# Performance work log

Measured on AMD Instinct MI355X. Metric: run time of the kernel, lower is better.

Reference implementation:

```python
import jax, jax.numpy as jnp
import numpy as np

B, C, H, W = 16, 256, 64, 64
HID, N, SD, NH, HD, NC = 256, 300, 64, 4, 16, 80


def _conv1x1(x, w, b):
    # x: (B,Cin,H,W), w: (Cout,Cin)
    return jnp.einsum('bchw,oc->bohw', x, w) + b[None, :, None, None]


def _lin(x, w, b):
    return x @ w.T + b


def _ln(x, g, b, eps=1e-5):
    mu = x.mean(-1, keepdims=True)
    var = ((x - mu) ** 2).mean(-1, keepdims=True)
    return (x - mu) / jnp.sqrt(var + eps) * g + b


def setup_inputs() -> dict:
    key = jax.random.key(0)
    ks = jax.random.split(key, 16)
    def w(k, shape, s=0.02):
        return jax.random.normal(k, shape, jnp.float32) * s
    return {
        'x': jax.random.normal(ks[0], (B, C, H, W), jnp.float32),
        'spotlight_sources': w(ks[1], (N, SD)),
        'pos_w': w(ks[2], (HID // 2, 2)), 'pos_b': jnp.zeros((HID // 2,), jnp.float32),
        'fp_w': w(ks[3], (HID, C)), 'fp_b': jnp.zeros((HID,), jnp.float32),
        'bn_g': jnp.ones((HID,), jnp.float32), 'bn_b': jnp.zeros((HID,), jnp.float32),
        'bn_m': jnp.zeros((HID,), jnp.float32), 'bn_v': jnp.ones((HID,), jnp.float32),
        'key_w': w(ks[4], (SD, HID)), 'key_b': jnp.zeros((SD,), jnp.float32),
        'val_w': w(ks[5], (HID, HID)), 'val_b': jnp.zeros((HID,), jnp.float32),
        'ctp_w': w(ks[6], (NC, HID)), 'ctp_b': jnp.zeros((NC,), jnp.float32),
        'bb1_w': w(ks[7], (HID, HID)), 'bb1_b': jnp.zeros((HID,), jnp.float32),
        'bbln_g': jnp.ones((HID,), jnp.float32), 'bbln_b': jnp.zeros((HID,), jnp.float32),
        'bb2_w': w(ks[8], (HID // 2, HID)), 'bb2_b': jnp.zeros((HID // 2,), jnp.float32),
        'bb3_w': w(ks[9], (4, HID // 2)), 'bb3_b': jnp.zeros((4,), jnp.float32),
        'ch1_w': w(ks[10], (HID, HID)), 'ch1_b': jnp.zeros((HID,), jnp.float32),
        'chln_g': jnp.ones((HID,), jnp.float32), 'chln_b': jnp.zeros((HID,), jnp.float32),
        'ch2_w': w(ks[11], (HID // 2, HID)), 'ch2_b': jnp.zeros((HID // 2,), jnp.float32),
        'ch3_w': w(ks[12], (1, HID // 2)), 'ch3_b': jnp.zeros((1,), jnp.float32),
    }


def _forward(x, spotlight_sources, pos_w, pos_b, fp_w, fp_b, bn_g, bn_b, bn_m, bn_v,
             key_w, key_b, val_w, val_b, ctp_w, ctp_b,
             bb1_w, bb1_b, bbln_g, bbln_b, bb2_w, bb2_b, bb3_w, bb3_b,
             ch1_w, ch1_b, chln_g, chln_b, ch2_w, ch2_b, ch3_w, ch3_b):
    Bv, _, Hh, Ww = x.shape
    # position encoding: 2-channel normalized (y, x) grid, conv1x1 to HID//2
    y = jnp.linspace(-1.0, 1.0, Hh, dtype=jnp.float32)
    xc = jnp.linspace(-1.0, 1.0, Ww, dtype=jnp.float32)
    coords = jnp.stack([jnp.broadcast_to(y[:, None], (Hh, Ww)),
                        jnp.broadcast_to(xc[None, :], (Hh, Ww))], 0)[None]  # (1,2,H,W)
    # feature_proj: conv1x1 + BatchNorm(eval) + ReLU
    feats = _conv1x1(x, fp_w, fp_b)
    feats = (feats - bn_m[None, :, None, None]) / jnp.sqrt(bn_v[None, :, None, None] + 1e-5)
    feats = jax.nn.relu(feats * bn_g[None, :, None, None] + bn_b[None, :, None, None])
    pos = jnp.broadcast_to(_conv1x1(coords, pos_w, pos_b), (Bv, HID // 2, Hh, Ww))
    comb = jnp.concatenate([feats[:, :HID // 2], pos], axis=1)  # (B,HID,H,W)
    keys = _conv1x1(comb, key_w, key_b).reshape(Bv, NH, HD, Hh * Ww)   # (B,h,d,M)
    vals = _conv1x1(comb, val_w, val_b).reshape(Bv, HID, Hh * Ww)      # (B,HID,M)
    q = spotlight_sources.reshape(N, NH, HD)                            # (N,h,d)
    logits = jnp.einsum('nhd,bhdm->bhnm', q, keys) / jnp.sqrt(jnp.float32(HD))
    attn = jax.nn.softmax(logits, axis=-1).mean(axis=1)                 # (B,N,M), head-averaged
    maps = attn.reshape(Bv, N, Hh, Ww)
    sf = jnp.einsum('bnm,bcm->bnc', attn, vals)                         # (B,N,HID)
    def head(z, w1, b1, g, bb, w2, b2, w3, b3):
        z = jax.nn.relu(_ln(_lin(z, w1, b1), g, bb))
        z = jax.nn.relu(_lin(z, w2, b2))
        return _lin(z, w3, b3)
    boxes = head(sf, bb1_w, bb1_b, bbln_g, bbln_b, bb2_w, bb2_b, bb3_w, bb3_b)
    scores = jax.nn.sigmoid(head(sf, ch1_w, ch1_b, chln_g, chln_b, ch2_w, ch2_b, ch3_w, ch3_b))
    cls = _lin(sf, ctp_w, ctp_b)
    # diversity loss: mean off-diagonal cosine similarity of attention rows
    an = attn / jnp.maximum(jnp.linalg.norm(attn, axis=2, keepdims=True), 1e-12)
    sim = jnp.einsum('bnm,bkm->bnk', an, an)
    div = (sim.sum() - jnp.einsum('bnn->', sim)) / (N * (N - 1)) * 0.1
    return boxes, scores, cls, maps, div, sf


def reference(x, spotlight_sources, pos_w, pos_b, fp_w, fp_b, bn_g, bn_b, bn_m, bn_v,
              key_w, key_b, val_w, val_b, ctp_w, ctp_b,
              bb1_w, bb1_b, bbln_g, bbln_b, bb2_w, bb2_b, bb3_w, bb3_b,
              ch1_w, ch1_b, chln_g, chln_b, ch2_w, ch2_b, ch3_w, ch3_b):
    return _forward(x, spotlight_sources, pos_w, pos_b, fp_w, fp_b, bn_g, bn_b, bn_m, bn_v,
                    key_w, key_b, val_w, val_b, ctp_w, ctp_b,
                    bb1_w, bb1_b, bbln_g, bbln_b, bb2_w, bb2_b, bb3_w, bb3_b,
                    ch1_w, ch1_b, chln_g, chln_b, ch2_w, ch2_b, ch3_w, ch3_b)
```

## Files before the change

### kernel.cpp

```cpp
#include <hip/hip_runtime.h>
#include <math.h>

#define BB 16
#define CIN 256
#define MM 4096
#define HIDC 256
#define NQ 300
#define NHH 4
#define HDD 16

#define OFF_BOXES  0
#define OFF_SCORES 19200
#define OFF_CLS    24000
#define OFF_MAPS   408000
#define OFF_DIV    20068800
#define OFF_SF     20068801

#define WS_COMB16  0
#define WS_KEYS16  8388608
#define WS_ATTN16  10485760
#define WS_T16     21544960
#define WS_VALW16  22159360
#define WS_SUMS    22192128
#define WS_NORM    22211328
#define WS_ACC     22216128
#define WS_P       22216192

#define HP_SF16   (WS_P + 0)
#define HP_Z2BB   (WS_P + 2457600)
#define HP_Z2CH   (WS_P + 2764800)
#define HP_HW     (WS_P + 3072000)
#define WS_B2     (WS_P + 3180544)
#define WS_Q16    (WS_P + 3200000)
#define WS_XT     25426432
#define WS_COMBT  33815040
#define WS_FPW16  42203648
#define WS_KEYW16 42220032
#define WS_Z1PRE2 42228224
#define WS_Z1B16  44685824

#define HW_BB1 0
#define HW_CH1 65536
#define HW_BB2 131072
#define HW_CH2 163840
#define HW_CTP 196608

typedef short short8 __attribute__((ext_vector_type(8)));
typedef float floatx4 __attribute__((ext_vector_type(4)));

__device__ __forceinline__ unsigned short f2bf(float f){
  unsigned int u = __float_as_uint(f);
  u = (u + 0x7FFFu + ((u >> 16) & 1u)) >> 16;
  return (unsigned short)u;
}
__device__ __forceinline__ float bf1(unsigned short u){
  return __uint_as_float((unsigned int)u << 16);
}

__global__ __launch_bounds__(256) void zero4_kernel(float4* __restrict__ p, int n4){
  int i = blockIdx.x * 256 + threadIdx.x;
  if (i < n4) p[i] = make_float4(0.f, 0.f, 0.f, 0.f);
}

__global__ __launch_bounds__(256) void init_kernel(const float* __restrict__ ss,
    const float* __restrict__ fp_w, const float* __restrict__ key_w,
    unsigned short* __restrict__ q16, unsigned short* __restrict__ fpw16,
    unsigned short* __restrict__ keyw16){
  int i = blockIdx.x * 256 + threadIdx.x;
  int T = gridDim.x * 256;
  for (int j = i; j < 320*64; j += T)
    q16[j] = (j < NQ*64) ? f2bf(ss[j] * 0.25f) : (unsigned short)0;
  for (int j = i; j < 128*256; j += T) fpw16[j] = f2bf(fp_w[j]);
  for (int j = i; j < 64*256; j += T)  keyw16[j] = f2bf(key_w[j]);
}

__global__ __launch_bounds__(256) void cast_heads_kernel(
    const float* __restrict__ val_w, const float* __restrict__ bb1_w,
    const float* __restrict__ ch1_w, const float* __restrict__ bb2_w,
    const float* __restrict__ ch2_w, const float* __restrict__ ctp_w,
    const float* __restrict__ bb2_b, const float* __restrict__ ch2_b,
    unsigned short* __restrict__ valw16, unsigned short* __restrict__ hw16,
    float* __restrict__ b2){
  int i = blockIdx.x * 256 + threadIdx.x;
  int T = gridDim.x * 256;
  for (int j = i; j < 65536; j += T) valw16[j] = f2bf(val_w[j]);
  for (int j = i; j < 65536; j += T) hw16[HW_BB1 + j] = f2bf(bb1_w[j]);
  for (int j = i; j < 65536; j += T) hw16[HW_CH1 + j] = f2bf(ch1_w[j]);
  for (int j = i; j < 32768; j += T) hw16[HW_BB2 + j] = f2bf(bb2_w[j]);
  for (int j = i; j < 32768; j += T) hw16[HW_CH2 + j] = f2bf(ch2_w[j]);
  for (int j = i; j < 20480; j += T) hw16[HW_CTP + j] = f2bf(ctp_w[j]);
  for (int j = i; j < 128; j += T){ b2[j] = bb2_b[j]; b2[128 + j] = ch2_b[j]; }
}

__global__ __launch_bounds__(256) void pos_kernel(const float* __restrict__ pos_w,
                                                  const float* __restrict__ pos_b,
                                                  unsigned short* __restrict__ comb16,
                                                  unsigned short* __restrict__ combT){
  int lin = blockIdx.x * 256 + threadIdx.x;
  if (lin < 2097152){
    int m  = (lin & 1023) * 4;
    int c  = (lin >> 10) & 127;
    int b  = lin >> 17;
    int row = m >> 6, col = m & 63;
    float y  = -1.f + 2.f * (float)row / 63.f;
    float wy = pos_w[c*2], wx = pos_w[c*2+1], pb = pos_b[c];
    float base = wy * y + pb;
    ushort4 u;
    u.x = f2bf(base + wx * (-1.f + 2.f * (float)(col+0) / 63.f));
    u.y = f2bf(base + wx * (-1.f + 2.f * (float)(col+1) / 63.f));
    u.z = f2bf(base + wx * (-1.f + 2.f * (float)(col+2) / 63.f));
    u.w = f2bf(base + wx * (-1.f + 2.f * (float)(col+3) / 63.f));
    *(ushort4*)&comb16[((size_t)(b*HIDC + 128 + c))*MM + m] = u;
  } else if (lin < 2097152 + 131072){
    int l2 = lin - 2097152;
    int c4 = (l2 & 31) * 4;
    int m  = l2 >> 5;
    int row = m >> 6, col = m & 63;
    float y = -1.f + 2.f * (float)row / 63.f;
    float x = -1.f + 2.f * (float)col / 63.f;
    ushort4 u;
    u.x = f2bf(pos_w[(c4+0)*2] * y + pos_w[(c4+0)*2+1] * x + pos_b[c4+0]);
    u.y = f2bf(pos_w[(c4+1)*2] * y + pos_w[(c4+1)*2+1] * x + pos_b[c4+1]);
    u.z = f2bf(pos_w[(c4+2)*2] * y + pos_w[(c4+2)*2+1] * x + pos_b[c4+2]);
    u.w = f2bf(pos_w[(c4+3)*2] * y + pos_w[(c4+3)*2+1] * x + pos_b[c4+3]);
    #pragma unroll
    for (int b = 0; b < BB; b++)
      *(ushort4*)&combT[((size_t)b*MM + m)*CIN + 128 + c4] = u;
  }
}

__global__ __launch_bounds__(256) void transpose_x_kernel(
    const float* __restrict__ in, unsigned short* __restrict__ outp){
  int b = blockIdx.z;
  int m0 = blockIdx.x * 64;
  int r0 = blockIdx.y * 64;
  __shared__ unsigned short lds[64][68];
  int t = threadIdx.x;
  const float* ib = in + (size_t)b * CIN * MM;
  #pragma unroll
  for (int j = 0; j < 4; j++){
    int lin = j*256 + t;
    int rr = lin >> 4;
    int m4 = (lin & 15) * 4;
    float4 v = *(const float4*)&ib[(size_t)(r0 + rr)*MM + m0 + m4];
    lds[m4+0][rr] = f2bf(v.x);
    lds[m4+1][rr] = f2bf(v.y);
    lds[m4+2][rr] = f2bf(v.z);
    lds[m4+3][rr] = f2bf(v.w);
  }
  __syncthreads();
  unsigned short* ob = outp + (size_t)b * MM * CIN;
  #pragma unroll
  for (int j = 0; j < 4; j++){
    int lin = j*256 + t;
    int mm = lin >> 4;
    int c4 = (lin & 15) * 4;
    ushort4 u;
    u.x = lds[mm][c4+0]; u.y = lds[mm][c4+1];
    u.z = lds[mm][c4+2]; u.w = lds[mm][c4+3];
    *(ushort4*)&ob[(size_t)(m0 + mm)*CIN + r0 + c4] = u;
  }
}

__global__ __launch_bounds__(64) void comb_mfma_kernel(
    const unsigned short* __restrict__ fpw16, const unsigned short* __restrict__ xT16,
    const float* __restrict__ fp_b, const float* __restrict__ bn_g,
    const float* __restrict__ bn_b, const float* __restrict__ bn_m,
    const float* __restrict__ bn_v, unsigned short* __restrict__ comb16,
    unsigned short* __restrict__ combT){
  int b = blockIdx.z;
  const unsigned short* Bb = xT16 + (size_t)b * MM * CIN;
  unsigned short* cb  = comb16 + (size_t)b * HIDC * MM;
  unsigned short* cTb = combT + (size_t)b * MM * CIN;
  int lane = threadIdx.x;
  int r16 = lane & 15;
  int ko  = (lane >> 4) * 8;
  const unsigned short* arow[4];
  const unsigned short* brow[4];
  #pragma unroll
  for (int i = 0; i < 4; i++){
    arow[i] = fpw16 + (size_t)(blockIdx.y*64 + i*16 + r16) * CIN + ko;
    brow[i] = Bb + (size_t)(blockIdx.x*64 + i*16 + r16) * CIN + ko;
  }
  floatx4 acc[4][4];
  #pragma unroll
  for (int i = 0; i < 4; i++)
    #pragma unroll
    for (int j = 0; j < 4; j++)
      acc[i][j] = (floatx4){0.f, 0.f, 0.f, 0.f};
  short8 a[4], bv[4], a2[4], b2[4];
  #pragma unroll
  for (int i = 0; i < 4; i++){
    a[i]  = *(const short8*)(arow[i]);
    bv[i] = *(const short8*)(brow[i]);
  }
  for (int k = 32; k < CIN; k += 32){
    #pragma unroll
    for (int i = 0; i < 4; i++){
      a2[i] = *(const short8*)(arow[i] + k);
      b2[i] = *(const short8*)(brow[i] + k);
    }
    #pragma unroll
    for (int i = 0; i < 4; i++)
      #pragma unroll
      for (int j = 0; j < 4; j++)
        acc[i][j] = __builtin_amdgcn_mfma_f32_16x16x32_bf16(a[i], bv[j], acc[i][j], 0, 0, 0);
    #pragma unroll
    for (int i = 0; i < 4; i++){ a[i] = a2[i]; bv[i] = b2[i]; }
  }
  #pragma unroll
  for (int i = 0; i < 4; i++)
    #pragma unroll
    for (int j = 0; j < 4; j++)
      acc[i][j] = __builtin_amdgcn_mfma_f32_16x16x32_bf16(a[i], bv[j], acc[i][j], 0, 0, 0);
  int cq = lane & 15, rq = (lane >> 4) * 4;
  #pragma unroll
  for (int i = 0; i < 4; i++){
    int rbase = blockIdx.y*64 + i*16 + rq;
    float mul[4], ofs[4];
    #pragma unroll
    for (int reg = 0; reg < 4; reg++){
      int rr = rbase + reg;
      float sc = rsqrtf(bn_v[rr] + 1e-5f);
      mul[reg] = sc * bn_g[rr];
      ofs[reg] = (fp_b[rr] - bn_m[rr]) * mul[reg] + bn_b[rr];
    }
    #pragma unroll
    for (int j = 0; j < 4; j++){
      int cc = blockIdx.x*64 + j*16 + cq;
      ushort4 u;
      float v0 = fmaxf(acc[i][j][0] * mul[0] + ofs[0], 0.f); u.x = f2bf(v0);
      float v1 = fmaxf(acc[i][j][1] * mul[1] + ofs[1], 0.f); u.y = f2bf(v1);
      float v2 = fmaxf(acc[i][j][2] * mul[2] + ofs[2], 0.f); u.z = f2bf(v2);
      float v3 = fmaxf(acc[i][j][3] * mul[3] + ofs[3], 0.f); u.w = f2bf(v3);
      cb[(size_t)(rbase+0) * MM + cc] = u.x;
      cb[(size_t)(rbase+1) * MM + cc] = u.y;
      cb[(size_t)(rbase+2) * MM + cc] = u.z;
      cb[(size_t)(rbase+3) * MM + cc] = u.w;
      *(ushort4*)&cTb[(size_t)cc * CIN + rbase] = u;
    }
  }
}


__global__ __launch_bounds__(256) void attn_sums_kernel(
    const unsigned short* __restrict__ q16, const unsigned short* __restrict__ keysT,
    float* __restrict__ sums){
  int b = blockIdx.z, ny = blockIdx.y, mx = blockIdx.x;
  int tid = threadIdx.x, w = tid >> 6, lane = tid & 63;
  int n0 = ny * 64;
  int l15 = lane & 15, qh = lane >> 4;
  int ko = (qh & 1) * 8;
  bool lo = lane < 32;
  const unsigned short* kT = keysT + (size_t)b * MM * 64;
  int mwb = mx*128 + w*32;
  __shared__ unsigned short qlds[64][72];
  __shared__ float spart[4][NHH][64];
  for (int c = tid; c < 512; c += 256){
    int r = c >> 3, d8 = (c & 7) * 8;
    *(short8*)&qlds[r][d8] = *(const short8*)&q16[(size_t)(n0 + r)*64 + d8];
  }
  __syncthreads();
  short8 zz = {0,0,0,0,0,0,0,0};
  #pragma unroll 1
  for (int h = 0; h < NHH; h++){
    short8 bq[4];
    #pragma unroll
    for (int ni = 0; ni < 4; ni++)
      bq[ni] = lo ? *(const short8*)&qlds[ni*16 + l15][h*16 + ko] : zz;
    float sacc[4] = {0.f, 0.f, 0.f, 0.f};
    #pragma unroll
    for (int ms = 0; ms < 2; ms++){
      int m = mwb + ms*16 + l15;
      short8 a = lo ? *(const short8*)&kT[(size_t)m*64 + h*16 + ko] : zz;
      #pragma unroll
      for (int ni = 0; ni < 4; ni++){
        floatx4 l = __builtin_amdgcn_mfma_f32_16x16x32_bf16(a, bq[ni],
                        (floatx4){0.f,0.f,0.f,0.f}, 0, 0, 0);
        sacc[ni] += __expf(l[0]) + __expf(l[1]) + __expf(l[2]) + __expf(l[3]);
      }
    }
    #pragma unroll
    for (int ni = 0; ni < 4; ni++){
      float v = sacc[ni];
      v += __shfl_xor(v, 16); v += __shfl_xor(v, 32);
      if (lane < 16) spart[w][h][ni*16 + lane] = v;
    }
  }
  __syncthreads();
  if (tid < NHH*64){
    int h = tid >> 6, r = tid & 63, n = n0 + r;
    if (n < NQ){
      float v = spart[0][h][r] + spart[1][h][r] + spart[2][h][r] + spart[3][h][r];
      atomicAdd(&sums[((size_t)b*NHH + h)*NQ + n], v);
    }
  }
}

__global__ __launch_bounds__(256) void attn_emit_kernel(
    const unsigned short* __restrict__ q16, const unsigned short* __restrict__ keysT,
    const float* __restrict__ sums, float* __restrict__ maps,
    unsigned short* __restrict__ attn16, float* __restrict__ norms){
  int b = blockIdx.z, ny = blockIdx.y, mx = blockIdx.x;
  int tid = threadIdx.x, w = tid >> 6, lane = tid & 63;
  int n0 = ny * 64;
  int l15 = lane & 15, qh = lane >> 4;
  int ko = (qh & 1) * 8;
  bool lo = lane < 32;
  __shared__ unsigned short qlds[64][72];
  __shared__ float inv_s[NHH][64];
  __shared__ float npart[4][64];
  for (int c = tid; c < 512; c += 256){
    int r = c >> 3, d8 = (c & 7) * 8;
    *(short8*)&qlds[r][d8] = *(const short8*)&q16[(size_t)(n0 + r)*64 + d8];
  }
  if (tid < NHH*64){
    int h = tid >> 6, r = tid & 63, n = n0 + r;
    inv_s[h][r] = (n < NQ) ? 0.25f / sums[((size_t)b*NHH + h)*NQ + n] : 0.f;
  }
  __syncthreads();
  const unsigned short* kT = keysT + (size_t)b * MM * 64;
  int mwb = mx*128 + w*32;
  short8 zz = {0,0,0,0,0,0,0,0};
  float nacc[4] = {0.f, 0.f, 0.f, 0.f};
  float* mb = maps + (size_t)b * NQ * MM;
  unsigned short* ab = attn16 + (size_t)b * NQ * MM;
  #pragma unroll 1
  for (int ms = 0; ms < 2; ms++){
    asm volatile("" ::: "memory");
    int mbase = mwb + ms*16;
    int mk = mbase + l15;
    floatx4 o[4];
    #pragma unroll
    for (int ni = 0; ni < 4; ni++) o[ni] = (floatx4){0.f,0.f,0.f,0.f};
    #pragma unroll
    for (int h = 0; h < NHH; h++){
      short8 a = lo ? *(const short8*)&kT[(size_t)mk*64 + h*16 + ko] : zz;
      #pragma unroll
      for (int ni = 0; ni < 4; ni++){
        short8 bq = lo ? *(const short8*)&qlds[ni*16 + l15][h*16 + ko] : zz;
        floatx4 l = __builtin_amdgcn_mfma_f32_16x16x32_bf16(a, bq,
                        (floatx4){0.f,0.f,0.f,0.f}, 0, 0, 0);
        float iv = inv_s[h][ni*16 + l15];
        o[ni][0] += __expf(l[0]) * iv;
        o[ni][1] += __expf(l[1]) * iv;
        o[ni][2] += __expf(l[2]) * iv;
        o[ni][3] += __expf(l[3]) * iv;
      }
    }
    #pragma unroll
    for (int ni = 0; ni < 4; ni++){
      nacc[ni] += o[ni][0]*o[ni][0] + o[ni][1]*o[ni][1]
                + o[ni][2]*o[ni][2] + o[ni][3]*o[ni][3];
      int n = n0 + ni*16 + l15;
      if (n < NQ){
        size_t off = (size_t)n*MM + mbase + qh*4;
        float4 v; v.x = o[ni][0]; v.y = o[ni][1]; v.z = o[ni][2]; v.w = o[ni][3];
        *(float4*)&mb[off] = v;
        ushort4 u;
        u.x = f2bf(v.x); u.y = f2bf(v.y); u.z = f2bf(v.z); u.w = f2bf(v.w);
        *(ushort4*)&ab[off] = u;
      }
    }
  }
  #pragma unroll
  for (int ni = 0; ni < 4; ni++){
    float v = nacc[ni];
    v += __shfl_xor(v, 16); v += __shfl_xor(v, 32);
    if (lane < 16) npart[w][ni*16 + lane] = v;
  }
  __syncthreads();
  if (tid < 64){
    int n = n0 + tid;
    if (n < NQ){
      float v = npart[0][tid] + npart[1][tid] + npart[2][tid] + npart[3][tid];
      atomicAdd(&norms[(size_t)b*NQ + n], v);
    }
  }
}

template<bool RELU>
__global__ __launch_bounds__(64) void mfma_nt_kernel(
    const unsigned short* __restrict__ A, size_t sA,
    const unsigned short* __restrict__ B, size_t sB,
    const float* __restrict__ bias, int bstride,
    float* __restrict__ C, unsigned short* __restrict__ C16,
    size_t sC, int ldc, int Mr, int Nc, int K){
  int bz = blockIdx.z;
  const unsigned short* Ab = A + (size_t)bz * sA;
  const unsigned short* Bb = B + (size_t)bz * sB;
  int lane = threadIdx.x;
  int r16 = lane & 15;
  int ko  = (lane >> 4) * 8;
  const unsigned short* arow[4];
  const unsigned short* brow[4];
  #pragma unroll
  for (int i = 0; i < 4; i++){
    int m = blockIdx.y*64 + i*16 + r16;
    if (m > Mr - 1) m = Mr - 1;
    arow[i] = Ab + (size_t)m * K + ko;
    int n = blockIdx.x*64 + i*16 + r16;
    if (n > Nc - 1) n = Nc - 1;
    brow[i] = Bb + (size_t)n * K + ko;
  }
  floatx4 acc[4][4];
  #pragma unroll
  for (int i = 0; i < 4; i++)
    #pragma unroll
    for (int j = 0; j < 4; j++)
      acc[i][j] = (floatx4){0.f, 0.f, 0.f, 0.f};
  short8 a[4], bv[4], a2[4], b2[4];
  #pragma unroll
  for (int i = 0; i < 4; i++){
    a[i]  = *(const short8*)(arow[i]);
    bv[i] = *(const short8*)(brow[i]);
  }
  for (int k = 32; k < K; k += 32){
    #pragma unroll
    for (int i = 0; i < 4; i++){
      a2[i] = *(const short8*)(arow[i] + k);
      b2[i] = *(const short8*)(brow[i] + k);
    }
    #pragma unroll
    for (int i = 0; i < 4; i++)
      #pragma unroll
      for (int j = 0; j < 4; j++)
        acc[i][j] = __builtin_amdgcn_mfma_f32_16x16x32_bf16(a[i], bv[j], acc[i][j], 0, 0, 0);
    #pragma unroll
    for (int i = 0; i < 4; i++){ a[i] = a2[i]; bv[i] = b2[i]; }
  }
  #pragma unroll
  for (int i = 0; i < 4; i++)
    #pragma unroll
    for (int j = 0; j < 4; j++)
      acc[i][j] = __builtin_amdgcn_mfma_f32_16x16x32_bf16(a[i], bv[j], acc[i][j], 0, 0, 0);
  int cq = lane & 15, rq = (lane >> 4) * 4;
  #pragma unroll
  for (int j = 0; j < 4; j++){
    int cc = blockIdx.x*64 + j*16 + cq;
    if (cc >= Nc) continue;
    float bv_ = bias ? bias[bz*bstride + cc] : 0.f;
    #pragma unroll
    for (int i = 0; i < 4; i++){
      int rbase = blockIdx.y*64 + i*16 + rq;
      #pragma unroll
      for (int reg = 0; reg < 4; reg++){
        int rr = rbase + reg;
        if (rr < Mr){
          float v = acc[i][j][reg] + bv_;
          if (RELU) v = fmaxf(v, 0.f);
          size_t o = (size_t)bz * sC + (size_t)rr * ldc + cc;
          if (C)   C[o] = v;
          if (C16) C16[o] = f2bf(v);
        }
      }
    }
  }
}

__global__ __launch_bounds__(256) void mfma_red4_kernel(
    const unsigned short* __restrict__ A, size_t sA,
    const unsigned short* __restrict__ B, size_t sB,
    unsigned short* __restrict__ C16, size_t sC, int ldc, int Mr, int K){
  int bz = blockIdx.z;
  int tid = threadIdx.x, w = tid >> 6, lane = tid & 63;
  int kchunk = K >> 2;
  const unsigned short* Ab = A + (size_t)bz * sA + (size_t)w * kchunk;
  const unsigned short* Bb = B + (size_t)bz * sB + (size_t)w * kchunk;
  int r16 = lane & 15;
  int ko  = (lane >> 4) * 8;
  const unsigned short* arow[4];
  const unsigned short* brow[4];
  #pragma unroll
  for (int i = 0; i < 4; i++){
    int m = blockIdx.y*64 + i*16 + r16;
    if (m > Mr - 1) m = Mr - 1;
    arow[i] = Ab + (size_t)m * K + ko;
    int n = blockIdx.x*64 + i*16 + r16;
    brow[i] = Bb + (size_t)n * K + ko;
  }
  floatx4 acc[4][4];
  #pragma unroll
  for (int i = 0; i < 4; i++)
    #pragma unroll
    for (int j = 0; j < 4; j++)
      acc[i][j] = (floatx4){0.f, 0.f, 0.f, 0.f};
  short8 a[4], bv[4], a2[4], b2[4];
  #pragma unroll
  for (int i = 0; i < 4; i++){
    a[i]  = *(const short8*)(arow[i]);
    bv[i] = *(const short8*)(brow[i]);
  }
  for (int k = 32; k < kchunk; k += 32){
    #pragma unroll
    for (int i = 0; i < 4; i++){
      a2[i] = *(const short8*)(arow[i] + k);
      b2[i] = *(const short8*)(brow[i] + k);
    }
    #pragma unroll
    for (int i = 0; i < 4; i++)
      #pragma unroll
      for (int j = 0; j < 4; j++)
        acc[i][j] = __builtin_amdgcn_mfma_f32_16x16x32_bf16(a[i], bv[j], acc[i][j], 0, 0, 0);
    #pragma unroll
    for (int i = 0; i < 4; i++){ a[i] = a2[i]; bv[i] = b2[i]; }
  }
  #pragma unroll
  for (int i = 0; i < 4; i++)
    #pragma unroll
    for (int j = 0; j < 4; j++)
      acc[i][j] = __builtin_amdgcn_mfma_f32_16x16x32_bf16(a[i], bv[j], acc[i][j], 0, 0, 0);
  __shared__ float red[64][65];
  int cq = lane & 15, rq = (lane >> 4) * 4;
  #pragma unroll 1
  for (int ph = 0; ph < 4; ph++){
    if (w == ph){
      #pragma unroll
      for (int i = 0; i < 4; i++)
        #pragma unroll
        for (int reg = 0; reg < 4; reg++){
          int r = i*16 + rq + reg;
          #pragma unroll
          for (int j = 0; j < 4; j++){
            int c = j*16 + cq;
            if (ph == 0) red[r][c] = acc[i][j][reg];
            else         red[r][c] += acc[i][j][reg];
          }
        }
    }
    __syncthreads();
  }
  unsigned short* Cb = C16 + (size_t)bz * sC;
  for (int idx = tid; idx < 1024; idx += 256){
    int r = idx >> 4, c4 = (idx & 15) * 4;
    int gr = blockIdx.y*64 + r;
    if (gr < Mr){
      ushort4 u;
      u.x = f2bf(red[r][c4+0]); u.y = f2bf(red[r][c4+1]);
      u.z = f2bf(red[r][c4+2]); u.w = f2bf(red[r][c4+3]);
      *(ushort4*)&Cb[(size_t)gr * ldc + blockIdx.x*64 + c4] = u;
    }
  }
}

__global__ __launch_bounds__(256) void ln_relu2_kernel(const float* __restrict__ zin,
    const float* __restrict__ bias_b, const float* __restrict__ bias_c,
    const float* __restrict__ g_b, const float* __restrict__ be_b,
    const float* __restrict__ g_c, const float* __restrict__ be_c,
    unsigned short* __restrict__ zout){
  int z = blockIdx.y;
  const float* bias = z ? bias_c : bias_b;
  const float* g    = z ? g_c : g_b;
  const float* be   = z ? be_c : be_b;
  const float* zi = zin + (size_t)z * 1228800;
  unsigned short* zo = zout + (size_t)z * 1228800;
  int row = blockIdx.x * 4 + (threadIdx.x >> 6);
  int lane = threadIdx.x & 63;
  float4 v = *(const float4*)&zi[(size_t)row * 256 + lane * 4];
  float4 bi = *(const float4*)&bias[lane * 4];
  v.x += bi.x; v.y += bi.y; v.z += bi.z; v.w += bi.w;
  float s = v.x + v.y + v.z + v.w;
  #pragma unroll
  for (int off = 32; off >= 1; off >>= 1) s += __shfl_xor(s, off);
  float mean = s * (1.f/256.f);
  float dx = v.x - mean, dy = v.y - mean, dz = v.z - mean, dw = v.w - mean;
  float sq = dx*dx + dy*dy + dz*dz + dw*dw;
  #pragma unroll
  for (int off = 32; off >= 1; off >>= 1) sq += __shfl_xor(sq, off);
  float inv = rsqrtf(sq * (1.f/256.f) + 1e-5f);
  float4 gv = *(const float4*)&g[lane * 4];
  float4 bb = *(const float4*)&be[lane * 4];
  ushort4 u;
  u.x = f2bf(fmaxf(dx*inv*gv.x + bb.x, 0.f));
  u.y = f2bf(fmaxf(dy*inv*gv.y + bb.y, 0.f));
  u.z = f2bf(fmaxf(dz*inv*gv.z + bb.z, 0.f));
  u.w = f2bf(fmaxf(dw*inv*gv.w + bb.w, 0.f));
  *(ushort4*)&zo[(size_t)row * 256 + lane * 4] = u;
}

__global__ __launch_bounds__(256) void head3_kernel(
    const unsigned short* __restrict__ z2bb, const unsigned short* __restrict__ z2ch,
    const float* __restrict__ bb3_w, const float* __restrict__ bb3_b,
    const float* __restrict__ ch3_w, const float* __restrict__ ch3_b,
    float* __restrict__ boxes, float* __restrict__ scores){
  int row = blockIdx.x * 4 + (threadIdx.x >> 6);
  int lane = threadIdx.x & 63;
  float zb0 = bf1(z2bb[(size_t)row*128 + 2*lane]);
  float zb1 = bf1(z2bb[(size_t)row*128 + 2*lane + 1]);
  float zc0 = bf1(z2ch[(size_t)row*128 + 2*lane]);
  float zc1 = bf1(z2ch[(size_t)row*128 + 2*lane + 1]);
  float acc[5];
  #pragma unroll
  for (int o = 0; o < 4; o++)
    acc[o] = bb3_w[o*128 + 2*lane]*zb0 + bb3_w[o*128 + 2*lane + 1]*zb1;
  acc[4] = ch3_w[2*lane]*zc0 + ch3_w[2*lane + 1]*zc1;
  #pragma unroll
  for (int o = 0; o < 5; o++){
    float v = acc[o];
    #pragma unroll
    for (int off = 32; off >= 1; off >>= 1) v += __shfl_xor(v, off);
    acc[o] = v;
  }
  if (lane == 0){
    #pragma unroll
    for (int o = 0; o < 4; o++)
      boxes[(size_t)row*4 + o] = acc[o] + bb3_b[o];
    float sv = acc[4] + ch3_b[0];
    scores[row] = 1.f / (1.f + __expf(-sv));
  }
}

__global__ __launch_bounds__(256) void simdiv_kernel(const unsigned short* __restrict__ attn16,
    const float* __restrict__ norms, float* __restrict__ acc){
  int b = blockIdx.y;
  int m = blockIdx.x * 256 + threadIdx.x;
  __shared__ float inv_s[NQ];
  __shared__ float red[4];
  for (int i = threadIdx.x; i < NQ; i += 256)
    inv_s[i] = 1.f / fmaxf(sqrtf(norms[(size_t)b * NQ + i]), 1e-12f);
  __syncthreads();
  const unsigned short* ab = attn16 + (size_t)b * NQ * MM;
  float S = 0.f;
  for (int n = 0; n < NQ; n++)
    S += bf1(ab[(size_t)n * MM + m]) * inv_s[n];
  float p = S * S;
  #pragma unroll
  for (int off = 32; off >= 1; off >>= 1) p += __shfl_xor(p, off);
  int w = threadIdx.x >> 6, lane = threadIdx.x & 63;
  if (lane == 0) red[w] = p;
  __syncthreads();
  if (threadIdx.x == 0) atomicAdd(acc, red[0] + red[1] + red[2] + red[3]);
}

__global__ void finalize_kernel(const float* __restrict__ acc, float* __restrict__ out_div){
  out_div[0] = (acc[0] - (float)(BB * NQ)) / (float)(NQ * (NQ - 1)) * 0.1f;
}

extern "C" void kernel_launch(void* const* d_in, const int* in_sizes, int n_in,
                              void* d_out, int out_size, void* d_ws, size_t ws_size,
                              hipStream_t stream){
  const float* x      = (const float*)d_in[0];
  const float* ss     = (const float*)d_in[1];
  const float* pos_w  = (const float*)d_in[2];
  const float* pos_b  = (const float*)d_in[3];
  const float* fp_w   = (const float*)d_in[4];
  const float* fp_b   = (const float*)d_in[5];
  const float* bn_g   = (const float*)d_in[6];
  const float* bn_b   = (const float*)d_in[7];
  const float* bn_m   = (const float*)d_in[8];
  const float* bn_v   = (const float*)d_in[9];
  const float* key_w  = (const float*)d_in[10];
  const float* key_b  = (const float*)d_in[11];
  const float* val_w  = (const float*)d_in[12];
  const float* val_b  = (const float*)d_in[13];
  const float* ctp_w  = (const float*)d_in[14];
  const float* ctp_b  = (const float*)d_in[15];
  const float* bb1_w  = (const float*)d_in[16];
  const float* bb1_b  = (const float*)d_in[17];
  const float* bbln_g = (const float*)d_in[18];
  const float* bbln_b = (const float*)d_in[19];
  const float* bb2_w  = (const float*)d_in[20];
  const float* bb2_b  = (const float*)d_in[21];
  const float* bb3_w  = (const float*)d_in[22];
  const float* bb3_b  = (const float*)d_in[23];
  const float* ch1_w  = (const float*)d_in[24];
  const float* ch1_b  = (const float*)d_in[25];
  const float* chln_g = (const float*)d_in[26];
  const float* chln_b = (const float*)d_in[27];
  const float* ch2_w  = (const float*)d_in[28];
  const float* ch2_b  = (const float*)d_in[29];
  const float* ch3_w  = (const float*)d_in[30];
  const float* ch3_b  = (const float*)d_in[31];

  float* out    = (float*)d_out;
  float* boxes  = out + OFF_BOXES;
  float* scores = out + OFF_SCORES;
  float* cls    = out + OFF_CLS;
  float* maps   = out + OFF_MAPS;
  float* divp   = out + OFF_DIV;
  float* sfout  = out + OFF_SF;

  float* ws = (float*)d_ws;
  unsigned short* comb16 = (unsigned short*)(ws + WS_COMB16);
  unsigned short* keysT  = (unsigned short*)(ws + WS_KEYS16);
  unsigned short* attn16 = (unsigned short*)(ws + WS_ATTN16);
  unsigned short* t16    = (unsigned short*)(ws + WS_T16);
  unsigned short* valw16 = (unsigned short*)(ws + WS_VALW16);
  float* sums  = ws + WS_SUMS;
  float* norms = ws + WS_NORM;
  float* dacc  = ws + WS_ACC;
  unsigned short* sf16   = (unsigned short*)(ws + HP_SF16);
  unsigned short* z2bb16 = (unsigned short*)(ws + HP_Z2BB);
  unsigned short* z2ch16 = (unsigned short*)(ws + HP_Z2CH);
  unsigned short* hw16   = (unsigned short*)(ws + HP_HW);
  float*          b2ws   = ws + WS_B2;
  unsigned short* q16    = (unsigned short*)(ws + WS_Q16);
  unsigned short* xT16   = (unsigned short*)(ws + WS_XT);
  unsigned short* combT  = (unsigned short*)(ws + WS_COMBT);
  unsigned short* fpw16  = (unsigned short*)(ws + WS_FPW16);
  unsigned short* keyw16 = (unsigned short*)(ws + WS_KEYW16);
  float*          z1pre2 = ws + WS_Z1PRE2;
  unsigned short* z1b16  = (unsigned short*)(ws + WS_Z1B16);

  zero4_kernel<<<24, 256, 0, stream>>>((float4*)sums, 6002);
  init_kernel<<<128, 256, 0, stream>>>(ss, fp_w, key_w, q16, fpw16, keyw16);

  transpose_x_kernel<<<dim3(64,4,16), 256, 0, stream>>>(x, xT16);
  pos_kernel<<<8704, 256, 0, stream>>>(pos_w, pos_b, comb16, combT);
  comb_mfma_kernel<<<dim3(64,2,16), 64, 0, stream>>>(
      fpw16, xT16, fp_b, bn_g, bn_b, bn_m, bn_v, comb16, combT);
  mfma_nt_kernel<false><<<dim3(1,64,16), 64, 0, stream>>>(
      combT, (size_t)MM*CIN, keyw16, 0, key_b, 0,
      nullptr, keysT, (size_t)MM*64, 64, MM, 64, CIN);

  attn_sums_kernel<<<dim3(32,5,16), 256, 0, stream>>>(q16, keysT, sums);
  attn_emit_kernel<<<dim3(32,5,16), 256, 0, stream>>>(q16, keysT, sums, maps, attn16, norms);

  mfma_red4_kernel<<<dim3(4,5,BB), 256, 0, stream>>>(
      attn16, (size_t)NQ*MM, comb16, (size_t)HIDC*MM,
      t16, (size_t)NQ*HIDC, HIDC, NQ, MM);
  cast_heads_kernel<<<256, 256, 0, stream>>>(val_w, bb1_w, ch1_w, bb2_w, ch2_w, ctp_w,
                                             bb2_b, ch2_b, valw16, hw16, b2ws);
  mfma_nt_kernel<false><<<dim3(4,5,BB), 64, 0, stream>>>(
      t16, (size_t)NQ*HIDC, valw16, 0, val_b, 0,
      sfout, sf16, (size_t)NQ*HIDC, HIDC, NQ, HIDC, HIDC);

  mfma_nt_kernel<false><<<dim3(4,75,2), 64, 0, stream>>>(
      sf16, 0, hw16 + HW_BB1, (size_t)(HW_CH1 - HW_BB1), nullptr, 0,
      z1pre2, nullptr, (size_t)4800*256, 256, 4800, 256, 256);
  ln_relu2_kernel<<<dim3(1200,2), 256, 0, stream>>>(
      z1pre2, bb1_b, ch1_b, bbln_g, bbln_b, chln_g, chln_b, z1b16);
  mfma_nt_kernel<true><<<dim3(2,75,2), 64, 0, stream>>>(
      z1b16, (size_t)4800*256, hw16 + HW_BB2, (size_t)(HW_CH2 - HW_BB2), b2ws, 128,
      nullptr, z2bb16, (size_t)4800*128, 128, 4800, 128, 256);
  head3_kernel<<<1200, 256, 0, stream>>>(z2bb16, z2ch16, bb3_w, bb3_b, ch3_w, ch3_b, boxes, scores);
  mfma_nt_kernel<false><<<dim3(2,75,1), 64, 0, stream>>>(
      sf16, 0, hw16 + HW_CTP, 0, ctp_b, 0, cls, nullptr, 0, 80, 4800, 80, 256);

  simdiv_kernel<<<dim3(16,16), 256, 0, stream>>>(attn16, norms, dacc);
  finalize_kernel<<<1, 1, 0, stream>>>(dacc, divp);
}
```

Measured before the change: 500.8 us.

## Replace in-block 4-way split-K attention GEMM with 8-way grid split-K plus reduce kernel

```diff
diff --git a/kernel.cpp b/kernel.cpp
--- a/kernel.cpp
+++ b/kernel.cpp
@@ -458,15 +458,16 @@
   }
 }
 
-__global__ __launch_bounds__(256) void mfma_red4_kernel(
+__global__ __launch_bounds__(64) void mfma_nt_splitk_kernel(
     const unsigned short* __restrict__ A, size_t sA,
     const unsigned short* __restrict__ B, size_t sB,
-    unsigned short* __restrict__ C16, size_t sC, int ldc, int Mr, int K){
-  int bz = blockIdx.z;
-  int tid = threadIdx.x, w = tid >> 6, lane = tid & 63;
-  int kchunk = K >> 2;
-  const unsigned short* Ab = A + (size_t)bz * sA + (size_t)w * kchunk;
-  const unsigned short* Bb = B + (size_t)bz * sB + (size_t)w * kchunk;
+    float* __restrict__ C, size_t sC, int ldc, int Mr, int K, int kchunk){
+  int nks = K / kchunk;
+  int bz = blockIdx.z / nks;
+  int kz = blockIdx.z % nks;
+  const unsigned short* Ab = A + (size_t)bz * sA + (size_t)kz * kchunk;
+  const unsigned short* Bb = B + (size_t)bz * sB + (size_t)kz * kchunk;
+  int lane = threadIdx.x;
   int r16 = lane & 15;
   int ko  = (lane >> 4) * 8;
   const unsigned short* arow[4];
@@ -510,36 +511,38 @@
     #pragma unroll
     for (int j = 0; j < 4; j++)
       acc[i][j] = __builtin_amdgcn_mfma_f32_16x16x32_bf16(a[i], bv[j], acc[i][j], 0, 0, 0);
-  __shared__ float red[64][65];
   int cq = lane & 15, rq = (lane >> 4) * 4;
-  #pragma unroll 1
-  for (int ph = 0; ph < 4; ph++){
-    if (w == ph){
+  #pragma unroll
+  for (int j = 0; j < 4; j++){
+    int cc = blockIdx.x*64 + j*16 + cq;
+    #pragma unroll
+    for (int i = 0; i < 4; i++){
+      int rbase = blockIdx.y*64 + i*16 + rq;
       #pragma unroll
-      for (int i = 0; i < 4; i++)
-        #pragma unroll
-        for (int reg = 0; reg < 4; reg++){
-          int r = i*16 + rq + reg;
-          #pragma unroll
-          for (int j = 0; j < 4; j++){
-            int c = j*16 + cq;
-            if (ph == 0) red[r][c] = acc[i][j][reg];
-            else         red[r][c] += acc[i][j][reg];
-          }
-        }
-    }
-    __syncthreads();
-  }
-  unsigned short* Cb = C16 + (size_t)bz * sC;
-  for (int idx = tid; idx < 1024; idx += 256){
-    int r = idx >> 4, c4 = (idx & 15) * 4;
-    int gr = blockIdx.y*64 + r;
-    if (gr < Mr){
-      ushort4 u;
-      u.x = f2bf(red[r][c4+0]); u.y = f2bf(red[r][c4+1]);
-      u.z = f2bf(red[r][c4+2]); u.w = f2bf(red[r][c4+3]);
-      *(ushort4*)&Cb[(size_t)gr * ldc + blockIdx.x*64 + c4] = u;
-    }
+      for (int reg = 0; reg < 4; reg++){
+        int rr = rbase + reg;
+        if (rr < Mr)
+          C[(size_t)blockIdx.z * sC + (size_t)rr * ldc + cc] = acc[i][j][reg];
+      }
+    }
+  }
+}
+
+__global__ __launch_bounds__(256) void cast_sum8_kernel(const float* __restrict__ part,
+                                                        unsigned short* __restrict__ dst, int n4){
+  int i = blockIdx.x * 256 + threadIdx.x;
+  if (i < n4){
+    int b = i / 19200, r = i - b * 19200;
+    const float4* p = (const float4*)part + (size_t)b * 8 * 19200 + r;
+    float4 s = p[0];
+    #pragma unroll
+    for (int k = 1; k < 8; k++){
+      float4 v = p[(size_t)k * 19200];
+      s.x += v.x; s.y += v.y; s.z += v.z; s.w += v.w;
+    }
+    ushort4 u;
+    u.x = f2bf(s.x); u.y = f2bf(s.y); u.z = f2bf(s.z); u.w = f2bf(s.w);
+    ((ushort4*)dst)[i] = u;
   }
 }
 
@@ -696,6 +699,7 @@
   float*          b2ws   = ws + WS_B2;
   unsigned short* q16    = (unsigned short*)(ws + WS_Q16);
   unsigned short* xT16   = (unsigned short*)(ws + WS_XT);
+  float*          tpart  = ws + WS_XT;
   unsigned short* combT  = (unsigned short*)(ws + WS_COMBT);
   unsigned short* fpw16  = (unsigned short*)(ws + WS_FPW16);
   unsigned short* keyw16 = (unsigned short*)(ws + WS_KEYW16);
@@ -716,9 +720,10 @@
   attn_sums_kernel<<<dim3(32,5,16), 256, 0, stream>>>(q16, keysT, sums);
   attn_emit_kernel<<<dim3(32,5,16), 256, 0, stream>>>(q16, keysT, sums, maps, attn16, norms);
 
-  mfma_red4_kernel<<<dim3(4,5,BB), 256, 0, stream>>>(
+  mfma_nt_splitk_kernel<<<dim3(4,5,BB*8), 64, 0, stream>>>(
       attn16, (size_t)NQ*MM, comb16, (size_t)HIDC*MM,
-      t16, (size_t)NQ*HIDC, HIDC, NQ, MM);
+      tpart, (size_t)NQ*HIDC, HIDC, NQ, MM, MM/8);
+  cast_sum8_kernel<<<1200, 256, 0, stream>>>(tpart, t16, 307200);
   cast_heads_kernel<<<256, 256, 0, stream>>>(val_w, bb1_w, ch1_w, bb2_w, ch2_w, ctp_w,
                                              bb2_b, ch2_b, valw16, hw16, b2ws);
   mfma_nt_kernel<false><<<dim3(4,5,BB), 64, 0, stream>>>(
```

Result: faster. 481.3 us (-3.9%).
